# Performance work log

Measured on AMD Instinct MI355X. Metric: run time of the kernel, lower is better.

Reference implementation:

```python
import jax, jax.numpy as jnp
import numpy as np

B, T, D, H, HD = 2, 2048, 1024, 16, 64
NEG_INF = jnp.float32(-1e30)


def setup_inputs() -> dict:
    key = jax.random.key(0)
    ks = jax.random.split(key, 6)
    scale = 0.02
    return {
        "x": jax.random.normal(ks[0], (B, T, D), dtype=jnp.float32),
        "Wq": jax.random.normal(ks[1], (H, D, HD), dtype=jnp.float32) * scale,
        "Wk": jax.random.normal(ks[2], (H, D, HD), dtype=jnp.float32) * scale,
        "Wv": jax.random.normal(ks[3], (H, D, HD), dtype=jnp.float32) * scale,
        "Wp": jax.random.normal(ks[4], (D, H * HD), dtype=jnp.float32) * scale,
        "bp": jnp.zeros((D,), dtype=jnp.float32),
    }


def reference(x, Wq, Wk, Wv, Wp, bp):
    # Per-head QKV projections (stacked over heads): [B,H,T,HD]
    q = jnp.einsum("btd,hde->bhte", x, Wq)
    k = jnp.einsum("btd,hde->bhte", x, Wk)
    v = jnp.einsum("btd,hde->bhte", x, Wv)
    # Scaled scores [B,H,T,T] with causal mask, stable softmax
    scores = jnp.einsum("bhte,bhse->bhts", q, k) * (HD ** -0.5)
    causal = jnp.tril(jnp.ones((T, T), dtype=bool))
    scores = jnp.where(causal, scores, NEG_INF)
    attn = jax.nn.softmax(scores, axis=-1)
    out = jnp.einsum("bhts,bhse->bhte", attn, v)
    # Concat heads: [B,T,H*HD], then output projection (torch Linear: y = x @ W.T + b)
    concat = out.transpose(0, 2, 1, 3).reshape(B, T, H * HD)
    return concat @ Wp.T + bp
```

## Files before the change

### kernel.cpp

```cpp
#include <hip/hip_runtime.h>
#include <hip/hip_bf16.h>

#define TSEQ 2048
#define DM   1024
#define NH   16
#define HDIM 64
#define NB   2
#define BT   (NB*TSEQ)
#define QSCALE 0.1803368801111204f

typedef __attribute__((ext_vector_type(8))) short bf16x8;
typedef __attribute__((ext_vector_type(4))) float f32x4;

union BF8 { bf16x8 v; ushort u[8]; };

static __device__ __forceinline__ ushort f2b(float x) {
    unsigned u = __float_as_uint(x);
    return (ushort)((u + 0x7fff + ((u >> 16) & 1)) >> 16);
}

static __device__ __forceinline__ unsigned cvtpk(float lo, float hi) {
    unsigned r;
    asm("v_cvt_pk_bf16_f32 %0, %1, %2" : "=v"(r) : "v"(lo), "v"(hi));
    return r;
}

static __device__ __forceinline__ float fmax3(float a, float b, float c) {
    return fmaxf(fmaxf(a, b), c);
}

static __device__ __forceinline__ void gload16(const void* g, void* l) {
    __builtin_amdgcn_global_load_lds((const __attribute__((address_space(1))) void*)g,
                                     (__attribute__((address_space(3))) void*)l, 16, 0, 0);
}

__global__ __launch_bounds__(256) void prep_kernel(const float* __restrict__ x,
                                                   const float* __restrict__ Wq,
                                                   const float* __restrict__ Wk,
                                                   const float* __restrict__ Wv,
                                                   const float* __restrict__ Wp,
                                                   ushort* __restrict__ xb,
                                                   ushort* __restrict__ wpb,
                                                   ushort* __restrict__ wtb) {
    __shared__ float tile[64][65];
    const int g = blockIdx.x, t = threadIdx.x;
    if (g < 2560) {
        const float* src = (g < 2048) ? x : Wp;
        ushort* dst = (g < 2048) ? xb : wpb;
        int i = ((g < 2048) ? g : (g - 2048)) * 256 + t;
        const float4* s = reinterpret_cast<const float4*>(src);
        float4 a = s[2*i], b = s[2*i+1];
        union { ushort u[8]; int4 v; } r;
        r.u[0]=f2b(a.x); r.u[1]=f2b(a.y); r.u[2]=f2b(a.z); r.u[3]=f2b(a.w);
        r.u[4]=f2b(b.x); r.u[5]=f2b(b.y); r.u[6]=f2b(b.z); r.u[7]=f2b(b.w);
        reinterpret_cast<int4*>(dst)[i] = r.v;
        return;
    }
    const int gb = g - 2560;
    const int k0 = (gb & 15) * 64;
    const int math = gb >> 4;
    const int mat = math >> 4, h = math & 15;
    const float* W = (mat == 0 ? Wq : (mat == 1 ? Wk : Wv)) + (size_t)h * DM * HDIM;
#pragma unroll
    for (int it = 0; it < 4; ++it) {
        int row = it*16 + (t>>4), c4 = (t&15)*4;
        float4 v = *reinterpret_cast<const float4*>(&W[(size_t)(k0+row)*HDIM + c4]);
        tile[row][c4+0]=v.x; tile[row][c4+1]=v.y; tile[row][c4+2]=v.z; tile[row][c4+3]=v.w;
    }
    __syncthreads();
    ushort* out = wtb + (size_t)(mat*NH + h) * (HDIM*DM);
#pragma unroll
    for (int it = 0; it < 4; ++it) {
        int n = it*16 + (t>>4), kc = (t&15)*4;
        union { ushort u[4]; uint2 v; } r;
#pragma unroll
        for (int j = 0; j < 4; ++j) r.u[j] = f2b(tile[kc+j][n]);
        *reinterpret_cast<uint2*>(&out[(size_t)n*DM + k0 + kc]) = r.v;
    }
}

template<int EPI>
__global__ __launch_bounds__(256) void gemm_bt(const ushort* __restrict__ A,
                                               const ushort* __restrict__ B,
                                               const float* __restrict__ bias,
                                               void* __restrict__ C) {
    __shared__ ushort As[128*64];
    __shared__ ushort Bs[128*64];
    const int tid = threadIdx.x;
    const int w = tid >> 6, l = tid & 63;
    const int lr = l & 15, lg = l >> 4;
    const int wr = (w >> 1) * 64, wc = (w & 1) * 64;
    const int cpx = (int)gridDim.x >> 3;
    const int wg = ((int)blockIdx.x & 7) * cpx + ((int)blockIdx.x >> 3);
    const int m0 = (wg & 31) * 128;
    const int n0 = (wg >> 5) * 128;
    const int srow = l >> 3;
    const int scol = (l & 7) * 8;

    f32x4 acc[4][4];
#pragma unroll
    for (int a = 0; a < 4; ++a)
#pragma unroll
        for (int b = 0; b < 4; ++b) acc[a][b] = {0.f, 0.f, 0.f, 0.f};

    for (int kc = 0; kc < DM/64; ++kc) {
        __syncthreads();
#pragma unroll
        for (int c = 0; c < 4; ++c) {
            int chunk = w*4 + c;
            int r = chunk*8 + srow;
            gload16(&A[(size_t)(m0+r)*DM + kc*64 + scol], &As[chunk*512]);
            gload16(&B[(size_t)(n0+r)*DM + kc*64 + scol], &Bs[chunk*512]);
        }
        __syncthreads();
#pragma unroll
        for (int kk = 0; kk < 2; ++kk) {
            bf16x8 af[4], bf[4];
#pragma unroll
            for (int mf = 0; mf < 4; ++mf)
                af[mf] = *reinterpret_cast<const bf16x8*>(&As[(wr + mf*16 + lr)*64 + kk*32 + lg*8]);
#pragma unroll
            for (int nf = 0; nf < 4; ++nf)
                bf[nf] = *reinterpret_cast<const bf16x8*>(&Bs[(wc + nf*16 + lr)*64 + kk*32 + lg*8]);
            __builtin_amdgcn_s_setprio(1);
#pragma unroll
            for (int mf = 0; mf < 4; ++mf)
#pragma unroll
                for (int nf = 0; nf < 4; ++nf)
                    acc[mf][nf] = __builtin_amdgcn_mfma_f32_16x16x32_bf16(
                        af[mf], bf[nf], acc[mf][nf], 0, 0, 0);
            __builtin_amdgcn_s_setprio(0);
        }
    }

    if (EPI == 0) {
        ushort* O = (ushort*)C;
#pragma unroll
        for (int mf = 0; mf < 4; ++mf) {
#pragma unroll
            for (int i = 0; i < 4; ++i) {
                int m = m0 + wr + mf*16 + lg*4 + i;
                int bq = m >> 11, t = m & (TSEQ - 1);
#pragma unroll
                for (int nf = 0; nf < 4; ++nf) {
                    int col = n0 + wc + nf*16 + lr;
                    int mat = col >> 10, hh = (col >> 6) & 15, e = col & 63;
                    float sc = (mat == 0) ? QSCALE : 1.0f;
                    O[((size_t)(mat*2*NH + bq*NH + hh))*(TSEQ*HDIM) + (size_t)t*HDIM + e] =
                        f2b(acc[mf][nf][i] * sc);
                }
            }
        }
    } else {
        float* O = (float*)C;
#pragma unroll
        for (int mf = 0; mf < 4; ++mf) {
#pragma unroll
            for (int i = 0; i < 4; ++i) {
                int m = m0 + wr + mf*16 + lg*4 + i;
#pragma unroll
                for (int nf = 0; nf < 4; ++nf) {
                    int col = n0 + wc + nf*16 + lr;
                    O[(size_t)m*DM + col] = acc[mf][nf][i] + bias[col];
                }
            }
        }
    }
}

__global__ __launch_bounds__(512) void attn_mfma(const ushort* __restrict__ qkvb,
                                                 ushort* __restrict__ concatb) {
    __shared__ ushort Ks[2][64*64];
    __shared__ ushort Vt[2][64*64];
    __shared__ ushort Ps[8][16*64];
    const int tid = threadIdx.x;
    const int w = tid >> 6, l = tid & 63;
    const int lr = l & 15, lg = l >> 4;
    const int g = blockIdx.x;
    const int bh = (g & 7) * 4 + ((g >> 3) & 3);
    const int p  = g >> 5;
    const int qtHI = 16 + p, qtLO = 15 - p;
    const int sub = w >> 2;
    const int ws  = w & 3;
    const int myqt = sub ? qtLO : qtHI;
    const int q0 = myqt * 64 + ws * 16;

    const ushort* Q = qkvb + (size_t)bh * (TSEQ*HDIM);
    const ushort* K = Q + (size_t)2*NH*TSEQ*HDIM;
    const ushort* V = K + (size_t)2*NH*TSEQ*HDIM;

    bf16x8 qf[2];
#pragma unroll
    for (int kk = 0; kk < 2; ++kk)
        qf[kk] = *reinterpret_cast<const bf16x8*>(&Q[(size_t)(q0 + lr)*HDIM + kk*32 + lg*8]);

    f32x4 acc[4];
    float mrow = -3e38f, lrow = 0.f;
#pragma unroll
    for (int nf = 0; nf < 4; ++nf) acc[nf] = {0.f, 0.f, 0.f, 0.f};

    ushort* PsW = &Ps[w][0];
    const int krow = tid >> 3;
    const int kchunk = (tid & 7) ^ ((tid >> 3) & 7);

    {
        gload16(&K[(size_t)krow*HDIM + kchunk*8], &Ks[0][tid*8]);
        BF8 a;
        a.v = *reinterpret_cast<const bf16x8*>(&V[(size_t)l*HDIM + w*8]);
#pragma unroll
        for (int j = 0; j < 8; ++j)
            Vt[0][(w*8 + j)*64 + ((l>>3) ^ j)*8 + (l&7)] = a.u[j];
        __syncthreads();
    }

    int cur = 0;
    for (int jt = 0; jt <= qtHI; ++jt) {
        const int nxt = cur ^ 1;
        const int s0 = jt * 64;
        const bool pref = (jt < qtHI);
        const bool active = (sub == 0) || (jt <= qtLO);
        BF8 ga;
        if (pref) {
            const int s0n = s0 + 64;
            gload16(&K[(size_t)(s0n + krow)*HDIM + kchunk*8], &Ks[nxt][tid*8]);
            ga.v = *reinterpret_cast<const bf16x8*>(&V[(size_t)(s0n + l)*HDIM + w*8]);
        }

        if (active) {
            f32x4 sT[4];
#pragma unroll
            for (int nf = 0; nf < 4; ++nf) sT[nf] = {0.f, 0.f, 0.f, 0.f};
#pragma unroll
            for (int kk = 0; kk < 2; ++kk) {
                bf16x8 kf[4];
#pragma unroll
                for (int nf = 0; nf < 4; ++nf)
                    kf[nf] = *reinterpret_cast<const bf16x8*>(
                        &Ks[cur][(nf*16 + lr)*64 + ((kk*4 + lg) ^ (lr&7))*8]);
                __builtin_amdgcn_s_setprio(1);
#pragma unroll
                for (int nf = 0; nf < 4; ++nf)
                    sT[nf] = __builtin_amdgcn_mfma_f32_16x16x32_bf16(kf[nf], qf[kk], sT[nf], 0, 0, 0);
                __builtin_amdgcn_s_setprio(0);
            }
            if (jt == myqt) {
                int qrow = q0 + lr;
#pragma unroll
                for (int nf = 0; nf < 4; ++nf) {
                    int kbase = s0 + nf*16 + lg*4;
#pragma unroll
                    for (int i = 0; i < 4; ++i)
                        if (kbase + i > qrow) sT[nf][i] = -1e30f;
                }
            }
            float g0 = fmax3(sT[0][0], sT[0][1], sT[0][2]);
            float g1 = fmax3(sT[0][3], sT[1][0], sT[1][1]);
            float g2 = fmax3(sT[1][2], sT[1][3], sT[2][0]);
            float g3 = fmax3(sT[2][1], sT[2][2], sT[2][3]);
            float g4 = fmax3(sT[3][0], sT[3][1], sT[3][2]);
            float tm = fmaxf(fmax3(fmax3(g0, g1, g2), g3, g4), sT[3][3]);
            tm = fmaxf(tm, __shfl_xor(tm, 16, 64));
            tm = fmaxf(tm, __shfl_xor(tm, 32, 64));
            if (__any(tm > mrow + 8.0f)) {
                float mnew = fmaxf(mrow, tm);
                float corr = exp2f(mrow - mnew);
                lrow *= corr;
#pragma unroll
                for (int nf = 0; nf < 4; ++nf)
#pragma unroll
                    for (int i = 0; i < 4; ++i) acc[nf][i] *= corr;
                mrow = mnew;
            }
            float ps = 0.f;
#pragma unroll
            for (int nf = 0; nf < 4; ++nf)
#pragma unroll
                for (int i = 0; i < 4; ++i) { sT[nf][i] = exp2f(sT[nf][i] - mrow); ps += sT[nf][i]; }
            ps += __shfl_xor(ps, 16, 64);
            ps += __shfl_xor(ps, 32, 64);
            lrow += ps;
#pragma unroll
            for (int nf = 0; nf < 4; ++nf) {
                uint2 pk;
                pk.x = cvtpk(sT[nf][0], sT[nf][1]);
                pk.y = cvtpk(sT[nf][2], sT[nf][3]);
                *reinterpret_cast<uint2*>(
                    &PsW[lr*64 + ((2*nf + (lg>>1)) ^ (lr&7))*8 + (lg&1)*4]) = pk;
            }
#pragma unroll
            for (int kk = 0; kk < 2; ++kk) {
                bf16x8 vf[4];
#pragma unroll
                for (int nf = 0; nf < 4; ++nf)
                    vf[nf] = *reinterpret_cast<const bf16x8*>(
                        &Vt[cur][(nf*16 + lr)*64 + ((kk*4 + lg) ^ (lr&7))*8]);
                bf16x8 pf = *reinterpret_cast<const bf16x8*>(
                    &PsW[lr*64 + ((kk*4 + lg) ^ (lr&7))*8]);
                __builtin_amdgcn_s_setprio(1);
#pragma unroll
                for (int nf = 0; nf < 4; ++nf)
                    acc[nf] = __builtin_amdgcn_mfma_f32_16x16x32_bf16(vf[nf], pf, acc[nf], 0, 0, 0);
                __builtin_amdgcn_s_setprio(0);
            }
        }

        if (pref) {
#pragma unroll
            for (int j = 0; j < 8; ++j)
                Vt[nxt][(w*8 + j)*64 + ((l>>3) ^ j)*8 + (l&7)] = ga.u[j];
        }
        __syncthreads();
        cur = nxt;
    }

    const int b = bh >> 4, h = bh & 15;
    {
        float inv = 1.0f / lrow;
        int t = q0 + lr;
        ushort* o = concatb + ((size_t)(b*TSEQ + t))*DM + h*HDIM;
#pragma unroll
        for (int nf = 0; nf < 4; ++nf) {
            uint2 pk;
            pk.x = cvtpk(acc[nf][0]*inv, acc[nf][1]*inv);
            pk.y = cvtpk(acc[nf][2]*inv, acc[nf][3]*inv);
            *reinterpret_cast<uint2*>(&o[nf*16 + lg*4]) = pk;
        }
    }
}

extern "C" void kernel_launch(void* const* d_in, const int* in_sizes, int n_in,
                              void* d_out, int out_size, void* d_ws, size_t ws_size,
                              hipStream_t stream) {
    const float* x  = (const float*)d_in[0];
    const float* Wq = (const float*)d_in[1];
    const float* Wk = (const float*)d_in[2];
    const float* Wv = (const float*)d_in[3];
    const float* Wp = (const float*)d_in[4];
    const float* bp = (const float*)d_in[5];
    float* out = (float*)d_out;

    ushort* ws   = (ushort*)d_ws;
    ushort* xb   = ws;
    ushort* wtb  = xb  + (size_t)BT*DM;
    ushort* wpb  = wtb + (size_t)3*NH*HDIM*DM;
    ushort* qkvb = wpb + (size_t)DM*DM;
    ushort* cb   = qkvb + (size_t)3*2*NH*TSEQ*HDIM;

    prep_kernel<<<dim3(3328), 256, 0, stream>>>(x, Wq, Wk, Wv, Wp, xb, wpb, wtb);
    gemm_bt<0><<<dim3(32*24), 256, 0, stream>>>(xb, wtb, nullptr, qkvb);
    attn_mfma<<<dim3(512), 512, 0, stream>>>(qkvb, cb);
    gemm_bt<1><<<dim3(32*8), 256, 0, stream>>>(cb, wpb, bp, out);
}
```

Before: 126.1 us.

## Process two KV tiles per barrier with quad-buffered K/V shared memory

The attention loop now handles K/V tiles in pairs. Each pair issues both QK^T MFMA groups back to back before the two softmax/PV steps, and it prefetches the next pair into a four-slot shared buffer. This halves the number of __syncthreads and gives the scheduler more independent MFMA work to overlap with the softmax math. Shared memory grows to 4 K and 4 V tiles, and keeping two score tiles live raises register pressure, which may lower occupancy or cause spills.

```diff
diff --git a/kernel.cpp b/kernel.cpp
--- a/kernel.cpp
+++ b/kernel.cpp
@@ -168,10 +168,97 @@
     }
 }
 
+static __device__ __forceinline__ void qk_tile(const ushort* __restrict__ Ksb,
+                                               const bf16x8* qf, f32x4* sT,
+                                               int lr, int lg) {
+#pragma unroll
+    for (int nf = 0; nf < 4; ++nf) sT[nf] = {0.f, 0.f, 0.f, 0.f};
+#pragma unroll
+    for (int kk = 0; kk < 2; ++kk) {
+        bf16x8 kf[4];
+#pragma unroll
+        for (int nf = 0; nf < 4; ++nf)
+            kf[nf] = *reinterpret_cast<const bf16x8*>(
+                &Ksb[(nf*16 + lr)*64 + ((kk*4 + lg) ^ (lr&7))*8]);
+        __builtin_amdgcn_s_setprio(1);
+#pragma unroll
+        for (int nf = 0; nf < 4; ++nf)
+            sT[nf] = __builtin_amdgcn_mfma_f32_16x16x32_bf16(kf[nf], qf[kk], sT[nf], 0, 0, 0);
+        __builtin_amdgcn_s_setprio(0);
+    }
+}
+
+static __device__ __forceinline__ void smpv_tile(const ushort* __restrict__ Vtb,
+                                                 ushort* __restrict__ PsW,
+                                                 f32x4* sT, f32x4* acc,
+                                                 float& mrow, float& lrow,
+                                                 int s0, int q0, bool diag,
+                                                 int lr, int lg) {
+    if (diag) {
+        int qrow = q0 + lr;
+#pragma unroll
+        for (int nf = 0; nf < 4; ++nf) {
+            int kbase = s0 + nf*16 + lg*4;
+#pragma unroll
+            for (int i = 0; i < 4; ++i)
+                if (kbase + i > qrow) sT[nf][i] = -1e30f;
+        }
+    }
+    float g0 = fmax3(sT[0][0], sT[0][1], sT[0][2]);
+    float g1 = fmax3(sT[0][3], sT[1][0], sT[1][1]);
+    float g2 = fmax3(sT[1][2], sT[1][3], sT[2][0]);
+    float g3 = fmax3(sT[2][1], sT[2][2], sT[2][3]);
+    float g4 = fmax3(sT[3][0], sT[3][1], sT[3][2]);
+    float tm = fmaxf(fmax3(fmax3(g0, g1, g2), g3, g4), sT[3][3]);
+    tm = fmaxf(tm, __shfl_xor(tm, 16, 64));
+    tm = fmaxf(tm, __shfl_xor(tm, 32, 64));
+    if (__any(tm > mrow + 8.0f)) {
+        float mnew = fmaxf(mrow, tm);
+        float corr = exp2f(mrow - mnew);
+        lrow *= corr;
+#pragma unroll
+        for (int nf = 0; nf < 4; ++nf)
+#pragma unroll
+            for (int i = 0; i < 4; ++i) acc[nf][i] *= corr;
+        mrow = mnew;
+    }
+    float ps = 0.f;
+#pragma unroll
+    for (int nf = 0; nf < 4; ++nf)
+#pragma unroll
+        for (int i = 0; i < 4; ++i) { sT[nf][i] = exp2f(sT[nf][i] - mrow); ps += sT[nf][i]; }
+    ps += __shfl_xor(ps, 16, 64);
+    ps += __shfl_xor(ps, 32, 64);
+    lrow += ps;
+#pragma unroll
+    for (int nf = 0; nf < 4; ++nf) {
+        uint2 pk;
+        pk.x = cvtpk(sT[nf][0], sT[nf][1]);
+        pk.y = cvtpk(sT[nf][2], sT[nf][3]);
+        *reinterpret_cast<uint2*>(
+            &PsW[lr*64 + ((2*nf + (lg>>1)) ^ (lr&7))*8 + (lg&1)*4]) = pk;
+    }
+#pragma unroll
+    for (int kk = 0; kk < 2; ++kk) {
+        bf16x8 vf[4];
+#pragma unroll
+        for (int nf = 0; nf < 4; ++nf)
+            vf[nf] = *reinterpret_cast<const bf16x8*>(
+                &Vtb[(nf*16 + lr)*64 + ((kk*4 + lg) ^ (lr&7))*8]);
+        bf16x8 pf = *reinterpret_cast<const bf16x8*>(
+            &PsW[lr*64 + ((kk*4 + lg) ^ (lr&7))*8]);
+        __builtin_amdgcn_s_setprio(1);
+#pragma unroll
+        for (int nf = 0; nf < 4; ++nf)
+            acc[nf] = __builtin_amdgcn_mfma_f32_16x16x32_bf16(vf[nf], pf, acc[nf], 0, 0, 0);
+        __builtin_amdgcn_s_setprio(0);
+    }
+}
+
 __global__ __launch_bounds__(512) void attn_mfma(const ushort* __restrict__ qkvb,
                                                  ushort* __restrict__ concatb) {
-    __shared__ ushort Ks[2][64*64];
-    __shared__ ushort Vt[2][64*64];
+    __shared__ ushort Ks[4][64*64];
+    __shared__ ushort Vt[4][64*64];
     __shared__ ushort Ps[8][16*64];
     const int tid = threadIdx.x;
     const int w = tid >> 6, l = tid & 63;
@@ -184,6 +271,7 @@
     const int ws  = w & 3;
     const int myqt = sub ? qtLO : qtHI;
     const int q0 = myqt * 64 + ws * 16;
+    const int ntiles = qtHI + 1;
 
     const ushort* Q = qkvb + (size_t)bh * (TSEQ*HDIM);
     const ushort* K = Q + (size_t)2*NH*TSEQ*HDIM;
@@ -205,112 +293,61 @@
 
     {
         gload16(&K[(size_t)krow*HDIM + kchunk*8], &Ks[0][tid*8]);
-        BF8 a;
-        a.v = *reinterpret_cast<const bf16x8*>(&V[(size_t)l*HDIM + w*8]);
-#pragma unroll
-        for (int j = 0; j < 8; ++j)
-            Vt[0][(w*8 + j)*64 + ((l>>3) ^ j)*8 + (l&7)] = a.u[j];
+        gload16(&K[(size_t)(64 + krow)*HDIM + kchunk*8], &Ks[1][tid*8]);
+        BF8 a0, a1;
+        a0.v = *reinterpret_cast<const bf16x8*>(&V[(size_t)l*HDIM + w*8]);
+        a1.v = *reinterpret_cast<const bf16x8*>(&V[(size_t)(64 + l)*HDIM + w*8]);
+#pragma unroll
+        for (int j = 0; j < 8; ++j) {
+            Vt[0][(w*8 + j)*64 + ((l>>3) ^ j)*8 + (l&7)] = a0.u[j];
+            Vt[1][(w*8 + j)*64 + ((l>>3) ^ j)*8 + (l&7)] = a1.u[j];
+        }
         __syncthreads();
     }
 
-    int cur = 0;
-    for (int jt = 0; jt <= qtHI; ++jt) {
-        const int nxt = cur ^ 1;
-        const int s0 = jt * 64;
-        const bool pref = (jt < qtHI);
-        const bool active = (sub == 0) || (jt <= qtLO);
-        BF8 ga;
-        if (pref) {
-            const int s0n = s0 + 64;
-            gload16(&K[(size_t)(s0n + krow)*HDIM + kchunk*8], &Ks[nxt][tid*8]);
-            ga.v = *reinterpret_cast<const bf16x8*>(&V[(size_t)(s0n + l)*HDIM + w*8]);
-        }
-
-        if (active) {
-            f32x4 sT[4];
-#pragma unroll
-            for (int nf = 0; nf < 4; ++nf) sT[nf] = {0.f, 0.f, 0.f, 0.f};
-#pragma unroll
-            for (int kk = 0; kk < 2; ++kk) {
-                bf16x8 kf[4];
-#pragma unroll
-                for (int nf = 0; nf < 4; ++nf)
-                    kf[nf] = *reinterpret_cast<const bf16x8*>(
-                        &Ks[cur][(nf*16 + lr)*64 + ((kk*4 + lg) ^ (lr&7))*8]);
-                __builtin_amdgcn_s_setprio(1);
-#pragma unroll
-                for (int nf = 0; nf < 4; ++nf)
-                    sT[nf] = __builtin_amdgcn_mfma_f32_16x16x32_bf16(kf[nf], qf[kk], sT[nf], 0, 0, 0);
-                __builtin_amdgcn_s_setprio(0);
-            }
-            if (jt == myqt) {
-                int qrow = q0 + lr;
-#pragma unroll
-                for (int nf = 0; nf < 4; ++nf) {
-                    int kbase = s0 + nf*16 + lg*4;
-#pragma unroll
-                    for (int i = 0; i < 4; ++i)
-                        if (kbase + i > qrow) sT[nf][i] = -1e30f;
-                }
-            }
-            float g0 = fmax3(sT[0][0], sT[0][1], sT[0][2]);
-            float g1 = fmax3(sT[0][3], sT[1][0], sT[1][1]);
-            float g2 = fmax3(sT[1][2], sT[1][3], sT[2][0]);
-            float g3 = fmax3(sT[2][1], sT[2][2], sT[2][3]);
-            float g4 = fmax3(sT[3][0], sT[3][1], sT[3][2]);
-            float tm = fmaxf(fmax3(fmax3(g0, g1, g2), g3, g4), sT[3][3]);
-            tm = fmaxf(tm, __shfl_xor(tm, 16, 64));
-            tm = fmaxf(tm, __shfl_xor(tm, 32, 64));
-            if (__any(tm > mrow + 8.0f)) {
-                float mnew = fmaxf(mrow, tm);
-                float corr = exp2f(mrow - mnew);
-                lrow *= corr;
-#pragma unroll
-                for (int nf = 0; nf < 4; ++nf)
-#pragma unroll
-                    for (int i = 0; i < 4; ++i) acc[nf][i] *= corr;
-                mrow = mnew;
-            }
-            float ps = 0.f;
-#pragma unroll
-            for (int nf = 0; nf < 4; ++nf)
-#pragma unroll
-                for (int i = 0; i < 4; ++i) { sT[nf][i] = exp2f(sT[nf][i] - mrow); ps += sT[nf][i]; }
-            ps += __shfl_xor(ps, 16, 64);
-            ps += __shfl_xor(ps, 32, 64);
-            lrow += ps;
-#pragma unroll
-            for (int nf = 0; nf < 4; ++nf) {
-                uint2 pk;
-                pk.x = cvtpk(sT[nf][0], sT[nf][1]);
-                pk.y = cvtpk(sT[nf][2], sT[nf][3]);
-                *reinterpret_cast<uint2*>(
-                    &PsW[lr*64 + ((2*nf + (lg>>1)) ^ (lr&7))*8 + (lg&1)*4]) = pk;
-            }
-#pragma unroll
-            for (int kk = 0; kk < 2; ++kk) {
-                bf16x8 vf[4];
-#pragma unroll
-                for (int nf = 0; nf < 4; ++nf)
-                    vf[nf] = *reinterpret_cast<const bf16x8*>(
-                        &Vt[cur][(nf*16 + lr)*64 + ((kk*4 + lg) ^ (lr&7))*8]);
-                bf16x8 pf = *reinterpret_cast<const bf16x8*>(
-                    &PsW[lr*64 + ((kk*4 + lg) ^ (lr&7))*8]);
-                __builtin_amdgcn_s_setprio(1);
-#pragma unroll
-                for (int nf = 0; nf < 4; ++nf)
-                    acc[nf] = __builtin_amdgcn_mfma_f32_16x16x32_bf16(vf[nf], pf, acc[nf], 0, 0, 0);
-                __builtin_amdgcn_s_setprio(0);
-            }
-        }
-
-        if (pref) {
+    const int npairs = (ntiles + 1) >> 1;
+    for (int jtp = 0; jtp < npairs; ++jtp) {
+        const int jtA = 2*jtp, jtB = jtA + 1;
+        const int bufA = (jtp & 1) << 1;
+        const bool prefA = (jtA + 2 < ntiles);
+        const bool prefB = (jtB + 2 < ntiles);
+        BF8 gA, gB;
+        if (prefA) {
+            const int s0n = (jtA + 2) * 64;
+            gload16(&K[(size_t)(s0n + krow)*HDIM + kchunk*8], &Ks[bufA^2][tid*8]);
+            gA.v = *reinterpret_cast<const bf16x8*>(&V[(size_t)(s0n + l)*HDIM + w*8]);
+        }
+        if (prefB) {
+            const int s0n = (jtB + 2) * 64;
+            gload16(&K[(size_t)(s0n + krow)*HDIM + kchunk*8], &Ks[(bufA^2)+1][tid*8]);
+            gB.v = *reinterpret_cast<const bf16x8*>(&V[(size_t)(s0n + l)*HDIM + w*8]);
+        }
+
+        const bool actA = (sub == 0) || (jtA <= qtLO);
+        const bool actB = (jtB < ntiles) && ((sub == 0) || (jtB <= qtLO));
+        if (actA && actB) {
+            f32x4 sA[4], sB[4];
+            qk_tile(Ks[bufA],     qf, sA, lr, lg);
+            qk_tile(Ks[bufA + 1], qf, sB, lr, lg);
+            smpv_tile(Vt[bufA],     PsW, sA, acc, mrow, lrow, jtA*64, q0, jtA == myqt, lr, lg);
+            smpv_tile(Vt[bufA + 1], PsW, sB, acc, mrow, lrow, jtB*64, q0, jtB == myqt, lr, lg);
+        } else if (actA) {
+            f32x4 sA[4];
+            qk_tile(Ks[bufA], qf, sA, lr, lg);
+            smpv_tile(Vt[bufA], PsW, sA, acc, mrow, lrow, jtA*64, q0, jtA == myqt, lr, lg);
+        }
+
+        if (prefA) {
 #pragma unroll
             for (int j = 0; j < 8; ++j)
-                Vt[nxt][(w*8 + j)*64 + ((l>>3) ^ j)*8 + (l&7)] = ga.u[j];
+                Vt[bufA^2][(w*8 + j)*64 + ((l>>3) ^ j)*8 + (l&7)] = gA.u[j];
+        }
+        if (prefB) {
+#pragma unroll
+            for (int j = 0; j < 8; ++j)
+                Vt[(bufA^2)+1][(w*8 + j)*64 + ((l>>3) ^ j)*8 + (l&7)] = gB.u[j];
         }
         __syncthreads();
-        cur = nxt;
     }
 
     const int b = bh >> 4, h = bh & 15;
```

Result: slower. 149.8 us (+18.8%).

## Software-pipeline attention so PV of previous tile overlaps current QK

Applied to the files above, without the earlier changes.

The attention loop is restructured so that each iteration computes QK^T for the current key tile and then runs the P·V MFMAs for the previous tile before doing the softmax. The V tile buffer is triple-buffered so the previous tile's V stays resident while the next one is prefetched. The goal is to interleave independent MFMA work with the softmax's exp and reduction chain and shorten dependency stalls. In exchange it adds 8 KB of LDS, more live registers, and a tail PV step after the loop.

```diff
diff --git a/kernel.cpp b/kernel.cpp
--- a/kernel.cpp
+++ b/kernel.cpp
@@ -168,10 +168,101 @@
     }
 }
 
+static __device__ __forceinline__ void qk_tile(const ushort* __restrict__ Ksb,
+                                               const bf16x8* qf, f32x4* sT,
+                                               int lr, int lg) {
+#pragma unroll
+    for (int nf = 0; nf < 4; ++nf) sT[nf] = {0.f, 0.f, 0.f, 0.f};
+#pragma unroll
+    for (int kk = 0; kk < 2; ++kk) {
+        bf16x8 kf[4];
+#pragma unroll
+        for (int nf = 0; nf < 4; ++nf)
+            kf[nf] = *reinterpret_cast<const bf16x8*>(
+                &Ksb[(nf*16 + lr)*64 + ((kk*4 + lg) ^ (lr&7))*8]);
+        __builtin_amdgcn_s_setprio(1);
+#pragma unroll
+        for (int nf = 0; nf < 4; ++nf)
+            sT[nf] = __builtin_amdgcn_mfma_f32_16x16x32_bf16(kf[nf], qf[kk], sT[nf], 0, 0, 0);
+        __builtin_amdgcn_s_setprio(0);
+    }
+}
+
+static __device__ __forceinline__ void pv_tile(const ushort* __restrict__ Vtb,
+                                               const ushort* __restrict__ PsW,
+                                               f32x4* acc, int lr, int lg) {
+#pragma unroll
+    for (int kk = 0; kk < 2; ++kk) {
+        bf16x8 vf[4];
+#pragma unroll
+        for (int nf = 0; nf < 4; ++nf)
+            vf[nf] = *reinterpret_cast<const bf16x8*>(
+                &Vtb[(nf*16 + lr)*64 + ((kk*4 + lg) ^ (lr&7))*8]);
+        bf16x8 pf = *reinterpret_cast<const bf16x8*>(
+            &PsW[lr*64 + ((kk*4 + lg) ^ (lr&7))*8]);
+        __builtin_amdgcn_s_setprio(1);
+#pragma unroll
+        for (int nf = 0; nf < 4; ++nf)
+            acc[nf] = __builtin_amdgcn_mfma_f32_16x16x32_bf16(vf[nf], pf, acc[nf], 0, 0, 0);
+        __builtin_amdgcn_s_setprio(0);
+    }
+}
+
+static __device__ __forceinline__ void sm_store(ushort* __restrict__ PsW,
+                                                f32x4* sT, f32x4* acc,
+                                                float& mrow, float& lrow,
+                                                int s0, int q0, bool diag,
+                                                int lr, int lg) {
+    if (diag) {
+        int qrow = q0 + lr;
+#pragma unroll
+        for (int nf = 0; nf < 4; ++nf) {
+            int kbase = s0 + nf*16 + lg*4;
+#pragma unroll
+            for (int i = 0; i < 4; ++i)
+                if (kbase + i > qrow) sT[nf][i] = -1e30f;
+        }
+    }
+    float g0 = fmax3(sT[0][0], sT[0][1], sT[0][2]);
+    float g1 = fmax3(sT[0][3], sT[1][0], sT[1][1]);
+    float g2 = fmax3(sT[1][2], sT[1][3], sT[2][0]);
+    float g3 = fmax3(sT[2][1], sT[2][2], sT[2][3]);
+    float g4 = fmax3(sT[3][0], sT[3][1], sT[3][2]);
+    float tm = fmaxf(fmax3(fmax3(g0, g1, g2), g3, g4), sT[3][3]);
+    tm = fmaxf(tm, __shfl_xor(tm, 16, 64));
+    tm = fmaxf(tm, __shfl_xor(tm, 32, 64));
+    if (__any(tm > mrow + 8.0f)) {
+        float mnew = fmaxf(mrow, tm);
+        float corr = exp2f(mrow - mnew);
+        lrow *= corr;
+#pragma unroll
+        for (int nf = 0; nf < 4; ++nf)
+#pragma unroll
+            for (int i = 0; i < 4; ++i) acc[nf][i] *= corr;
+        mrow = mnew;
+    }
+    float ps = 0.f;
+#pragma unroll
+    for (int nf = 0; nf < 4; ++nf)
+#pragma unroll
+        for (int i = 0; i < 4; ++i) { sT[nf][i] = exp2f(sT[nf][i] - mrow); ps += sT[nf][i]; }
+    ps += __shfl_xor(ps, 16, 64);
+    ps += __shfl_xor(ps, 32, 64);
+    lrow += ps;
+#pragma unroll
+    for (int nf = 0; nf < 4; ++nf) {
+        uint2 pk;
+        pk.x = cvtpk(sT[nf][0], sT[nf][1]);
+        pk.y = cvtpk(sT[nf][2], sT[nf][3]);
+        *reinterpret_cast<uint2*>(
+            &PsW[lr*64 + ((2*nf + (lg>>1)) ^ (lr&7))*8 + (lg&1)*4]) = pk;
+    }
+}
+
 __global__ __launch_bounds__(512) void attn_mfma(const ushort* __restrict__ qkvb,
                                                  ushort* __restrict__ concatb) {
     __shared__ ushort Ks[2][64*64];
-    __shared__ ushort Vt[2][64*64];
+    __shared__ ushort Vt[3][64*64];
     __shared__ ushort Ps[8][16*64];
     const int tid = threadIdx.x;
     const int w = tid >> 6, l = tid & 63;
@@ -184,6 +275,7 @@
     const int ws  = w & 3;
     const int myqt = sub ? qtLO : qtHI;
     const int q0 = myqt * 64 + ws * 16;
+    const int ntiles = qtHI + 1;
 
     const ushort* Q = qkvb + (size_t)bh * (TSEQ*HDIM);
     const ushort* K = Q + (size_t)2*NH*TSEQ*HDIM;
@@ -214,11 +306,13 @@
     }
 
     int cur = 0;
-    for (int jt = 0; jt <= qtHI; ++jt) {
+    bool pend = false;
+    for (int jt = 0; jt < ntiles; ++jt) {
         const int nxt = cur ^ 1;
         const int s0 = jt * 64;
-        const bool pref = (jt < qtHI);
-        const bool active = (sub == 0) || (jt <= qtLO);
+        const bool pref = (jt + 1 < ntiles);
+        const int vwr = (jt + 1) % 3;
+        const int vrd = (jt + 2) % 3;
         BF8 ga;
         if (pref) {
             const int s0n = s0 + 64;
@@ -226,92 +320,29 @@
             ga.v = *reinterpret_cast<const bf16x8*>(&V[(size_t)(s0n + l)*HDIM + w*8]);
         }
 
+        const bool active = (sub == 0) || (jt <= qtLO);
         if (active) {
             f32x4 sT[4];
-#pragma unroll
-            for (int nf = 0; nf < 4; ++nf) sT[nf] = {0.f, 0.f, 0.f, 0.f};
-#pragma unroll
-            for (int kk = 0; kk < 2; ++kk) {
-                bf16x8 kf[4];
-#pragma unroll
-                for (int nf = 0; nf < 4; ++nf)
-                    kf[nf] = *reinterpret_cast<const bf16x8*>(
-                        &Ks[cur][(nf*16 + lr)*64 + ((kk*4 + lg) ^ (lr&7))*8]);
-                __builtin_amdgcn_s_setprio(1);
-#pragma unroll
-                for (int nf = 0; nf < 4; ++nf)
-                    sT[nf] = __builtin_amdgcn_mfma_f32_16x16x32_bf16(kf[nf], qf[kk], sT[nf], 0, 0, 0);
-                __builtin_amdgcn_s_setprio(0);
-            }
-            if (jt == myqt) {
-                int qrow = q0 + lr;
-#pragma unroll
-                for (int nf = 0; nf < 4; ++nf) {
-                    int kbase = s0 + nf*16 + lg*4;
-#pragma unroll
-                    for (int i = 0; i < 4; ++i)
-                        if (kbase + i > qrow) sT[nf][i] = -1e30f;
-                }
-            }
-            float g0 = fmax3(sT[0][0], sT[0][1], sT[0][2]);
-            float g1 = fmax3(sT[0][3], sT[1][0], sT[1][1]);
-            float g2 = fmax3(sT[1][2], sT[1][3], sT[2][0]);
-            float g3 = fmax3(sT[2][1], sT[2][2], sT[2][3]);
-            float g4 = fmax3(sT[3][0], sT[3][1], sT[3][2]);
-            float tm = fmaxf(fmax3(fmax3(g0, g1, g2), g3, g4), sT[3][3]);
-            tm = fmaxf(tm, __shfl_xor(tm, 16, 64));
-            tm = fmaxf(tm, __shfl_xor(tm, 32, 64));
-            if (__any(tm > mrow + 8.0f)) {
-                float mnew = fmaxf(mrow, tm);
-                float corr = exp2f(mrow - mnew);
-                lrow *= corr;
-#pragma unroll
-                for (int nf = 0; nf < 4; ++nf)
-#pragma unroll
-                    for (int i = 0; i < 4; ++i) acc[nf][i] *= corr;
-                mrow = mnew;
-            }
-            float ps = 0.f;
-#pragma unroll
-            for (int nf = 0; nf < 4; ++nf)
-#pragma unroll
-                for (int i = 0; i < 4; ++i) { sT[nf][i] = exp2f(sT[nf][i] - mrow); ps += sT[nf][i]; }
-            ps += __shfl_xor(ps, 16, 64);
-            ps += __shfl_xor(ps, 32, 64);
-            lrow += ps;
-#pragma unroll
-            for (int nf = 0; nf < 4; ++nf) {
-                uint2 pk;
-                pk.x = cvtpk(sT[nf][0], sT[nf][1]);
-                pk.y = cvtpk(sT[nf][2], sT[nf][3]);
-                *reinterpret_cast<uint2*>(
-                    &PsW[lr*64 + ((2*nf + (lg>>1)) ^ (lr&7))*8 + (lg&1)*4]) = pk;
-            }
-#pragma unroll
-            for (int kk = 0; kk < 2; ++kk) {
-                bf16x8 vf[4];
-#pragma unroll
-                for (int nf = 0; nf < 4; ++nf)
-                    vf[nf] = *reinterpret_cast<const bf16x8*>(
-                        &Vt[cur][(nf*16 + lr)*64 + ((kk*4 + lg) ^ (lr&7))*8]);
-                bf16x8 pf = *reinterpret_cast<const bf16x8*>(
-                    &PsW[lr*64 + ((kk*4 + lg) ^ (lr&7))*8]);
-                __builtin_amdgcn_s_setprio(1);
-#pragma unroll
-                for (int nf = 0; nf < 4; ++nf)
-                    acc[nf] = __builtin_amdgcn_mfma_f32_16x16x32_bf16(vf[nf], pf, acc[nf], 0, 0, 0);
-                __builtin_amdgcn_s_setprio(0);
-            }
+            qk_tile(Ks[cur], qf, sT, lr, lg);
+            if (pend)
+                pv_tile(Vt[vrd], PsW, acc, lr, lg);
+            sm_store(PsW, sT, acc, mrow, lrow, s0, q0, jt == myqt, lr, lg);
+            pend = true;
+        } else if (pend) {
+            pv_tile(Vt[vrd], PsW, acc, lr, lg);
+            pend = false;
         }
 
         if (pref) {
 #pragma unroll
             for (int j = 0; j < 8; ++j)
-                Vt[nxt][(w*8 + j)*64 + ((l>>3) ^ j)*8 + (l&7)] = ga.u[j];
+                Vt[vwr][(w*8 + j)*64 + ((l>>3) ^ j)*8 + (l&7)] = ga.u[j];
         }
         __syncthreads();
         cur = nxt;
     }
+    if (pend)
+        pv_tile(Vt[(ntiles + 2) % 3], PsW, acc, lr, lg);
 
     const int b = bh >> 4, h = bh & 15;
     {
```

New measurement: 128.3 us. No clear change (+1.8%).
